# Optimization experiments

Measured on AMD Instinct MI355X. Metric: run time of the kernel, lower is better.

Reference implementation:

```python
import jax, jax.numpy as jnp
import numpy as np


def _chord_mask(n):
    # Chord-protocol sparsity: mask[i, i] = 1 and mask[i, (i + 2**j) % n] = 1
    m = np.zeros((n, n), dtype=np.float32)
    idx = np.arange(n)
    m[idx, idx] = 1.0
    for j in range(int(np.log2(n))):
        m[idx, (idx + 2 ** j) % n] = 1.0
    return jnp.asarray(m)


def setup_inputs() -> dict:
    key = jax.random.key(0)
    ks = jax.random.split(key, 8)
    B, n_vec, n_dim = 16, 1024, 64
    n_hidden, n_W, n_class = 32, 10, 10
    data = jax.random.normal(ks[0], (B, n_vec, n_dim), dtype=jnp.float32)
    s1 = 1.0 / np.sqrt(n_dim)
    s2 = 1.0 / np.sqrt(n_hidden)
    s3 = 1.0 / np.sqrt(n_vec * n_dim)
    fW1 = jax.random.uniform(ks[1], (n_W, n_dim, n_hidden), jnp.float32, -s1, s1)
    fb1 = jax.random.uniform(ks[2], (n_W, n_hidden), jnp.float32, -s1, s1)
    fW2 = jax.random.uniform(ks[3], (n_W, n_hidden, n_vec), jnp.float32, -s2, s2)
    fb2 = jax.random.uniform(ks[4], (n_W, n_vec), jnp.float32, -s2, s2)
    final_W = jax.random.uniform(ks[5], (n_vec * n_dim, n_class), jnp.float32, -s3, s3)
    final_b = jax.random.uniform(ks[6], (n_class,), jnp.float32, -s3, s3)
    return {"data": data, "fW1": fW1, "fb1": fb1, "fW2": fW2, "fb2": fb2,
            "final_W": final_W, "final_b": final_b}


def reference(data, fW1, fb1, fW2, fb2, final_W, final_b):
    B, n_vec, n_dim = data.shape
    n_W = fW1.shape[0]
    mask = _chord_mask(n_vec)  # [n_vec, n_vec], static constant
    V = data
    residual = V
    # fs[::-1] -> iterate layers in reverse order
    for i in range(n_W - 1, -1, -1):
        h = jax.nn.gelu(jnp.einsum('bnd,dh->bnh', data, fW1[i]) + fb1[i],
                        approximate=False)
        W = jnp.einsum('bnh,hm->bnm', h, fW2[i]) + fb2[i]  # [B, n_vec, n_vec]
        W = W * mask
        V = jnp.einsum('bnm,bmd->bnd', W, V) + residual
        residual = V  # residual_every=True
    flat = V.reshape(B, n_vec * n_dim)
    return flat @ final_W + final_b
```

## Files before the change

kernel.cpp:

```cpp
#include <hip/hip_runtime.h>

#define BATCH 16
#define NVEC 1024
#define NDIM 64
#define NHID 32
#define NW   10
#define NCLS 10
#define NOFF 11
#define WPAD 12
#define NCHUNK (NDIM / 4)
#define W2PAD 36
#define NROW 8
#define NSLOT 64

__global__ __launch_bounds__(128, 2) void k_weights(
    const float* __restrict__ data,
    const float* __restrict__ fW1,
    const float* __restrict__ fb1,
    const float* __restrict__ fW2,
    const float* __restrict__ fb2,
    float* __restrict__ Wsp)
{
    const int i = blockIdx.y;
    const int nbase = blockIdx.x * NROW;
    const int t = threadIdx.x;
    const int jq = t & 3;
    const int b  = (t >> 2) & 15;
    const int nl = t >> 6;
    const int j0 = jq * 8;

    __shared__ __align__(16) float sW1[NDIM * NHID];
    __shared__ float sb1[NHID];
    __shared__ __align__(16) float sW2r[NSLOT * W2PAD];
    __shared__ float sb2[NSLOT];
    __shared__ __align__(16) float rws[NROW * BATCH * WPAD];

    {
        const float4* w1v = (const float4*)(fW1 + (size_t)i * NDIM * NHID);
        float4* s4 = (float4*)sW1;
        for (int k = t; k < NDIM * NHID / 4; k += 128) s4[k] = w1v[k];
        if (t < NHID) sb1[t] = fb1[i * NHID + t];

        const int s  = t & 63;
        const int j2 = t >> 6;
        int k = (s < 24) ? s : ((32 << ((s - 24) >> 3)) + ((s - 24) & 7));
        int m = (nbase + k) & (NVEC - 1);
        const float* w2 = fW2 + (size_t)i * NHID * NVEC + m;
        #pragma unroll 1
        for (int jj = 0; jj < 16; ++jj)
            sW2r[s * W2PAD + (j2 + jj * 2)] = w2[(size_t)(j2 + jj * 2) * NVEC];
        if (t < NSLOT) sb2[s] = fb2[(size_t)i * NVEC + m];

        rws[t * WPAD + (WPAD - 1)] = 0.0f;
    }
    __syncthreads();

    float h[4][8];
    #pragma unroll
    for (int r = 0; r < 4; ++r)
        #pragma unroll
        for (int jj = 0; jj < 8; ++jj) h[r][jj] = sb1[j0 + jj];

    const int n0 = nbase + nl * 4;
    const float4* rowp = (const float4*)(data + ((size_t)(b * NVEC) + n0) * NDIM);

    float4 c0 = rowp[0], c1 = rowp[16], c2 = rowp[32], c3 = rowp[48];
    #pragma unroll 1
    for (int g = 0; g < 16; ++g) {
        const int gn = (g + 1) & 15;
        float4 p0 = rowp[gn];
        float4 p1 = rowp[16 + gn];
        float4 p2 = rowp[32 + gn];
        float4 p3 = rowp[48 + gn];
        const float as0[4] = {c0.x, c0.y, c0.z, c0.w};
        const float as1[4] = {c1.x, c1.y, c1.z, c1.w};
        const float as2[4] = {c2.x, c2.y, c2.z, c2.w};
        const float as3[4] = {c3.x, c3.y, c3.z, c3.w};
        #pragma unroll
        for (int dk = 0; dk < 4; ++dk) {
            const float4* wp = (const float4*)(&sW1[(g * 4 + dk) * NHID + j0]);
            float4 w0 = wp[0], w1 = wp[1];
            const float wf[8] = {w0.x, w0.y, w0.z, w0.w, w1.x, w1.y, w1.z, w1.w};
            #pragma unroll
            for (int jj = 0; jj < 8; ++jj) {
                h[0][jj] += as0[dk] * wf[jj];
                h[1][jj] += as1[dk] * wf[jj];
                h[2][jj] += as2[dk] * wf[jj];
                h[3][jj] += as3[dk] * wf[jj];
            }
        }
        c0 = p0; c1 = p1; c2 = p2; c3 = p3;
    }

    #pragma unroll
    for (int r = 0; r < 4; ++r)
        #pragma unroll
        for (int jj = 0; jj < 8; ++jj) {
            float x = h[r][jj];
            h[r][jj] = 0.5f * x * (1.0f + erff(x * 0.70710678118654752f));
        }

    const int rbase = nl * 4;
    #pragma unroll 1
    for (int o = 0; o < NOFF; ++o) {
        const int off   = (o == 0) ? 0 : (1 << (o - 1));
        const int sbase = (o == 0) ? 0 : ((off <= 16) ? off : (24 + 8 * (o - 6)));
        const bool mine = (jq == (o & 3));
        #pragma unroll
        for (int r = 0; r < 4; ++r) {
            const int slot = sbase + rbase + r;
            const float4* gp = (const float4*)(sW2r + slot * W2PAD + j0);
            float4 g0 = gp[0], g1 = gp[1];
            float w = h[r][0] * g0.x + h[r][1] * g0.y + h[r][2] * g0.z + h[r][3] * g0.w
                    + h[r][4] * g1.x + h[r][5] * g1.y + h[r][6] * g1.z + h[r][7] * g1.w;
            w += __shfl_xor(w, 1, 64);
            w += __shfl_xor(w, 2, 64);
            if (mine)
                rws[(b * NROW + rbase + r) * WPAD + o] = w + sb2[slot];
        }
    }
    __syncthreads();

    {
        const float4* rv = (const float4*)rws;
        #pragma unroll 1
        for (int k = t; k < NROW * BATCH * 3; k += 128) {
            int row = k / 3, comp = k - row * 3;
            int bb = row >> 3, rr = row & 7;
            float4* dst = (float4*)(Wsp +
                ((size_t)(i * BATCH + bb) * NVEC + nbase + rr) * WPAD + comp * 4);
            *dst = rv[k];
        }
    }
}

__global__ __launch_bounds__(512) void k_chain(
    const float* __restrict__ data,
    const float* __restrict__ Wsp,
    const float* __restrict__ Wf,
    float* __restrict__ part)
{
    const int lin   = blockIdx.x;
    const int xcd   = lin & 7;
    const int slot  = lin >> 3;
    const int b     = (xcd << 1) | (slot >> 4);
    const int chunk = slot & 15;
    const int d0    = chunk * 4;
    const int n     = threadIdx.x;
    const int n2    = n + 512;

    __shared__ float4 bufA[NVEC];
    __shared__ float4 bufB[NVEC];

    float4 v0own = *(const float4*)(data + ((size_t)(b * NVEC) + n)  * NDIM + d0);
    float4 v1own = *(const float4*)(data + ((size_t)(b * NVEC) + n2) * NDIM + d0);
    bufA[n]  = v0own;
    bufA[n2] = v1own;

    const float* wbase = Wsp + (size_t)((NW - 1) * BATCH + b) * NVEC * WPAD;
    const float4* wp0 = (const float4*)(wbase + (size_t)n  * WPAD);
    const float4* wp1 = (const float4*)(wbase + (size_t)n2 * WPAD);
    float4 wa0 = wp0[0], wb0 = wp0[1], wc0 = wp0[2];
    float4 wa1 = wp1[0], wb1 = wp1[1], wc1 = wp1[2];
    __syncthreads();

    float4* cur = bufA;
    float4* nxt = bufB;

    for (int l = 0; l < NW; ++l) {
        float4 na0, nb0, nc0, na1, nb1, nc1;
        if (l < NW - 1) {
            const float* nbase_p = Wsp + (size_t)((NW - 2 - l) * BATCH + b) * NVEC * WPAD;
            const float4* q0 = (const float4*)(nbase_p + (size_t)n  * WPAD);
            const float4* q1 = (const float4*)(nbase_p + (size_t)n2 * WPAD);
            na0 = q0[0]; nb0 = q0[1]; nc0 = q0[2];
            na1 = q1[0]; nb1 = q1[1]; nc1 = q1[2];
        }
        const float wg0[12] = {wa0.x, wa0.y, wa0.z, wa0.w,
                               wb0.x, wb0.y, wb0.z, wb0.w,
                               wc0.x, wc0.y, wc0.z, wc0.w};
        const float wg1[12] = {wa1.x, wa1.y, wa1.z, wa1.w,
                               wb1.x, wb1.y, wb1.z, wb1.w,
                               wc1.x, wc1.y, wc1.z, wc1.w};
        float4 acc0;
        acc0.x = v0own.x + wg0[0] * v0own.x;
        acc0.y = v0own.y + wg0[0] * v0own.y;
        acc0.z = v0own.z + wg0[0] * v0own.z;
        acc0.w = v0own.w + wg0[0] * v0own.w;
        #pragma unroll
        for (int o = 1; o < NOFF; ++o) {
            int off = 1 << (o - 1);
            float4 vv = (off == 512) ? v1own : cur[(n + off) & (NVEC - 1)];
            acc0.x += wg0[o] * vv.x; acc0.y += wg0[o] * vv.y;
            acc0.z += wg0[o] * vv.z; acc0.w += wg0[o] * vv.w;
        }
        float4 acc1;
        acc1.x = v1own.x + wg1[0] * v1own.x;
        acc1.y = v1own.y + wg1[0] * v1own.y;
        acc1.z = v1own.z + wg1[0] * v1own.z;
        acc1.w = v1own.w + wg1[0] * v1own.w;
        #pragma unroll
        for (int o = 1; o < NOFF; ++o) {
            int off = 1 << (o - 1);
            float4 vv = (off == 512) ? v0own : cur[(n2 + off) & (NVEC - 1)];
            acc1.x += wg1[o] * vv.x; acc1.y += wg1[o] * vv.y;
            acc1.z += wg1[o] * vv.z; acc1.w += wg1[o] * vv.w;
        }
        nxt[n]  = acc0;
        nxt[n2] = acc1;
        v0own = acc0;
        v1own = acc1;
        __syncthreads();
        float4* tmp = cur; cur = nxt; nxt = tmp;
        if (l < NW - 1) {
            wa0 = na0; wb0 = nb0; wc0 = nc0;
            wa1 = na1; wb1 = nb1; wc1 = nc1;
        }
    }

    float p0[NCLS], p1[NCLS];
    #pragma unroll
    for (int c = 0; c < NCLS; ++c) { p0[c] = 0.0f; p1[c] = 0.0f; }
    {
        float vs0[4] = {v0own.x, v0own.y, v0own.z, v0own.w};
        float vs1[4] = {v1own.x, v1own.y, v1own.z, v1own.w};
        const float4* wfv0 = (const float4*)(Wf + ((size_t)(n  * NDIM + d0)) * NCLS);
        const float4* wfv1 = (const float4*)(Wf + ((size_t)(n2 * NDIM + d0)) * NCLS);
        float wf0[40], wf1[40];
        #pragma unroll
        for (int k = 0; k < 10; ++k) {
            float4 u0 = wfv0[k], u1 = wfv1[k];
            wf0[k * 4 + 0] = u0.x; wf0[k * 4 + 1] = u0.y;
            wf0[k * 4 + 2] = u0.z; wf0[k * 4 + 3] = u0.w;
            wf1[k * 4 + 0] = u1.x; wf1[k * 4 + 1] = u1.y;
            wf1[k * 4 + 2] = u1.z; wf1[k * 4 + 3] = u1.w;
        }
        #pragma unroll
        for (int d = 0; d < 4; ++d)
            #pragma unroll
            for (int cls = 0; cls < NCLS; ++cls) {
                p0[cls] += vs0[d] * wf0[d * NCLS + cls];
                p1[cls] += vs1[d] * wf1[d * NCLS + cls];
            }
    }

    const int lane = n & 63, wv = n >> 6;
    float* sred = (float*)nxt;
    #pragma unroll
    for (int cls = 0; cls < NCLS; ++cls) {
        float v0 = p0[cls];
        float v1 = p1[cls];
        #pragma unroll
        for (int s = 32; s > 0; s >>= 1) {
            v0 += __shfl_down(v0, s, 64);
            v1 += __shfl_down(v1, s, 64);
        }
        if (lane == 0) {
            sred[wv * NCLS + cls]       = v0;
            sred[(wv + 8) * NCLS + cls] = v1;
        }
    }
    __syncthreads();
    if (n < NCLS) {
        float s = 0.0f;
        #pragma unroll
        for (int w = 0; w < 16; ++w) s += sred[w * NCLS + n];
        part[(size_t)(b * NCHUNK + chunk) * NCLS + n] = s;
    }
}

__global__ __launch_bounds__(256) void k_finish(
    const float* __restrict__ part, const float* __restrict__ bias,
    float* __restrict__ out)
{
    int t = threadIdx.x;
    if (t < BATCH * NCLS) {
        int b = t / NCLS, cls = t % NCLS;
        float s = bias[cls];
        #pragma unroll
        for (int ch = 0; ch < NCHUNK; ++ch)
            s += part[(size_t)(b * NCHUNK + ch) * NCLS + cls];
        out[t] = s;
    }
}

extern "C" void kernel_launch(void* const* d_in, const int* in_sizes, int n_in,
                              void* d_out, int out_size, void* d_ws, size_t ws_size,
                              hipStream_t stream) {
    const float* data = (const float*)d_in[0];
    const float* fW1  = (const float*)d_in[1];
    const float* fb1  = (const float*)d_in[2];
    const float* fW2  = (const float*)d_in[3];
    const float* fb2  = (const float*)d_in[4];
    const float* fWf  = (const float*)d_in[5];
    const float* fbf  = (const float*)d_in[6];
    float* out = (float*)d_out;

    float* ws   = (float*)d_ws;
    float* Wsp  = ws;
    float* part = Wsp + (size_t)NW * BATCH * NVEC * WPAD;

    k_weights<<<dim3(NVEC / NROW, NW), 128, 0, stream>>>(
        data, fW1, fb1, fW2, fb2, Wsp);
    k_chain<<<dim3(NCHUNK * BATCH), 512, 0, stream>>>(data, Wsp, fWf, part);
    k_finish<<<dim3(1), 256, 0, stream>>>(part, fbf, out);
}
```

Before: 116.4 us.

## Split chain kernel into 2-column chunks and fold finish into atomics

The chain kernel now has each block handle 2 feature columns instead of 4, doubling the grid from 256 to 512 blocks so more CUs get work. It also halves per-thread registers and shared memory. The separate finish kernel is removed: the weights kernel writes the bias into the output, and each chain block atomically adds its partial class sums. This saves one launch, but every block now re-reads the full sparse weight rows, so weight traffic doubles, and float atomics make the summation order nondeterministic.

```diff
diff --git a/kernel.cpp b/kernel.cpp
--- a/kernel.cpp
+++ b/kernel.cpp
@@ -8,10 +8,10 @@
 #define NCLS 10
 #define NOFF 11
 #define WPAD 12
-#define NCHUNK (NDIM / 4)
 #define W2PAD 36
 #define NROW 8
 #define NSLOT 64
+#define NCHUNK2 32
 
 __global__ __launch_bounds__(128, 2) void k_weights(
     const float* __restrict__ data,
@@ -19,7 +19,9 @@
     const float* __restrict__ fb1,
     const float* __restrict__ fW2,
     const float* __restrict__ fb2,
-    float* __restrict__ Wsp)
+    float* __restrict__ Wsp,
+    const float* __restrict__ bias,
+    float* __restrict__ out)
 {
     const int i = blockIdx.y;
     const int nbase = blockIdx.x * NROW;
@@ -34,6 +36,10 @@
     __shared__ __align__(16) float sW2r[NSLOT * W2PAD];
     __shared__ float sb2[NSLOT];
     __shared__ __align__(16) float rws[NROW * BATCH * WPAD];
+
+    if (blockIdx.x == 0 && i == 0) {
+        for (int k = t; k < BATCH * NCLS; k += 128) out[k] = bias[k % NCLS];
+    }
 
     {
         const float4* w1v = (const float4*)(fW1 + (size_t)i * NDIM * NHID);
@@ -138,22 +144,22 @@
     const float* __restrict__ data,
     const float* __restrict__ Wsp,
     const float* __restrict__ Wf,
-    float* __restrict__ part)
+    float* __restrict__ out)
 {
     const int lin   = blockIdx.x;
     const int xcd   = lin & 7;
     const int slot  = lin >> 3;
-    const int b     = (xcd << 1) | (slot >> 4);
-    const int chunk = slot & 15;
-    const int d0    = chunk * 4;
+    const int b     = (xcd << 1) | (slot >> 5);
+    const int chunk = slot & 31;
+    const int d0    = chunk * 2;
     const int n     = threadIdx.x;
     const int n2    = n + 512;
 
-    __shared__ float4 bufA[NVEC];
-    __shared__ float4 bufB[NVEC];
-
-    float4 v0own = *(const float4*)(data + ((size_t)(b * NVEC) + n)  * NDIM + d0);
-    float4 v1own = *(const float4*)(data + ((size_t)(b * NVEC) + n2) * NDIM + d0);
+    __shared__ float2 bufA[NVEC];
+    __shared__ float2 bufB[NVEC];
+
+    float2 v0own = *(const float2*)(data + ((size_t)(b * NVEC) + n)  * NDIM + d0);
+    float2 v1own = *(const float2*)(data + ((size_t)(b * NVEC) + n2) * NDIM + d0);
     bufA[n]  = v0own;
     bufA[n2] = v1own;
 
@@ -164,8 +170,8 @@
     float4 wa1 = wp1[0], wb1 = wp1[1], wc1 = wp1[2];
     __syncthreads();
 
-    float4* cur = bufA;
-    float4* nxt = bufB;
+    float2* cur = bufA;
+    float2* nxt = bufB;
 
     for (int l = 0; l < NW; ++l) {
         float4 na0, nb0, nc0, na1, nb1, nc1;
@@ -182,36 +188,30 @@
         const float wg1[12] = {wa1.x, wa1.y, wa1.z, wa1.w,
                                wb1.x, wb1.y, wb1.z, wb1.w,
                                wc1.x, wc1.y, wc1.z, wc1.w};
-        float4 acc0;
+        float2 acc0;
         acc0.x = v0own.x + wg0[0] * v0own.x;
         acc0.y = v0own.y + wg0[0] * v0own.y;
-        acc0.z = v0own.z + wg0[0] * v0own.z;
-        acc0.w = v0own.w + wg0[0] * v0own.w;
         #pragma unroll
         for (int o = 1; o < NOFF; ++o) {
             int off = 1 << (o - 1);
-            float4 vv = (off == 512) ? v1own : cur[(n + off) & (NVEC - 1)];
+            float2 vv = (off == 512) ? v1own : cur[(n + off) & (NVEC - 1)];
             acc0.x += wg0[o] * vv.x; acc0.y += wg0[o] * vv.y;
-            acc0.z += wg0[o] * vv.z; acc0.w += wg0[o] * vv.w;
-        }
-        float4 acc1;
+        }
+        float2 acc1;
         acc1.x = v1own.x + wg1[0] * v1own.x;
         acc1.y = v1own.y + wg1[0] * v1own.y;
-        acc1.z = v1own.z + wg1[0] * v1own.z;
-        acc1.w = v1own.w + wg1[0] * v1own.w;
         #pragma unroll
         for (int o = 1; o < NOFF; ++o) {
             int off = 1 << (o - 1);
-            float4 vv = (off == 512) ? v0own : cur[(n2 + off) & (NVEC - 1)];
+            float2 vv = (off == 512) ? v0own : cur[(n2 + off) & (NVEC - 1)];
             acc1.x += wg1[o] * vv.x; acc1.y += wg1[o] * vv.y;
-            acc1.z += wg1[o] * vv.z; acc1.w += wg1[o] * vv.w;
         }
         nxt[n]  = acc0;
         nxt[n2] = acc1;
         v0own = acc0;
         v1own = acc1;
         __syncthreads();
-        float4* tmp = cur; cur = nxt; nxt = tmp;
+        float2* tmp = cur; cur = nxt; nxt = tmp;
         if (l < NW - 1) {
             wa0 = na0; wb0 = nb0; wc0 = nc0;
             wa1 = na1; wb1 = nb1; wc1 = nc1;
@@ -222,21 +222,21 @@
     #pragma unroll
     for (int c = 0; c < NCLS; ++c) { p0[c] = 0.0f; p1[c] = 0.0f; }
     {
-        float vs0[4] = {v0own.x, v0own.y, v0own.z, v0own.w};
-        float vs1[4] = {v1own.x, v1own.y, v1own.z, v1own.w};
         const float4* wfv0 = (const float4*)(Wf + ((size_t)(n  * NDIM + d0)) * NCLS);
         const float4* wfv1 = (const float4*)(Wf + ((size_t)(n2 * NDIM + d0)) * NCLS);
-        float wf0[40], wf1[40];
-        #pragma unroll
-        for (int k = 0; k < 10; ++k) {
+        float wf0[20], wf1[20];
+        #pragma unroll
+        for (int k = 0; k < 5; ++k) {
             float4 u0 = wfv0[k], u1 = wfv1[k];
             wf0[k * 4 + 0] = u0.x; wf0[k * 4 + 1] = u0.y;
             wf0[k * 4 + 2] = u0.z; wf0[k * 4 + 3] = u0.w;
             wf1[k * 4 + 0] = u1.x; wf1[k * 4 + 1] = u1.y;
             wf1[k * 4 + 2] = u1.z; wf1[k * 4 + 3] = u1.w;
         }
-        #pragma unroll
-        for (int d = 0; d < 4; ++d)
+        const float vs0[2] = {v0own.x, v0own.y};
+        const float vs1[2] = {v1own.x, v1own.y};
+        #pragma unroll
+        for (int d = 0; d < 2; ++d)
             #pragma unroll
             for (int cls = 0; cls < NCLS; ++cls) {
                 p0[cls] += vs0[d] * wf0[d * NCLS + cls];
@@ -265,22 +265,7 @@
         float s = 0.0f;
         #pragma unroll
         for (int w = 0; w < 16; ++w) s += sred[w * NCLS + n];
-        part[(size_t)(b * NCHUNK + chunk) * NCLS + n] = s;
-    }
-}
-
-__global__ __launch_bounds__(256) void k_finish(
-    const float* __restrict__ part, const float* __restrict__ bias,
-    float* __restrict__ out)
-{
-    int t = threadIdx.x;
-    if (t < BATCH * NCLS) {
-        int b = t / NCLS, cls = t % NCLS;
-        float s = bias[cls];
-        #pragma unroll
-        for (int ch = 0; ch < NCHUNK; ++ch)
-            s += part[(size_t)(b * NCHUNK + ch) * NCLS + cls];
-        out[t] = s;
+        atomicAdd(out + b * NCLS + n, s);
     }
 }
 
@@ -298,10 +283,8 @@
 
     float* ws   = (float*)d_ws;
     float* Wsp  = ws;
-    float* part = Wsp + (size_t)NW * BATCH * NVEC * WPAD;
 
     k_weights<<<dim3(NVEC / NROW, NW), 128, 0, stream>>>(
-        data, fW1, fb1, fW2, fb2, Wsp);
-    k_chain<<<dim3(NCHUNK * BATCH), 512, 0, stream>>>(data, Wsp, fWf, part);
-    k_finish<<<dim3(1), 256, 0, stream>>>(part, fbf, out);
+        data, fW1, fb1, fW2, fb2, Wsp, fbf, out);
+    k_chain<<<dim3(NCHUNK2 * BATCH), 512, 0, stream>>>(data, Wsp, fWf, out);
 }
```

Measured after the change: 117.4 us. Within noise of the previous version (+0.9%).
